# Performance work log

Measured on AMD Instinct MI355X. Metric: run time of the kernel, lower is better.

The kernel has to match this reference:

```python
import jax, jax.numpy as jnp
import numpy as np

T, B, H, L = 512, 128, 256, 2  # seq_len, batch, hidden(=input) size, num_layers


def setup_inputs() -> dict:
    key = jax.random.key(0)
    k0, k1, k2, k3, k4 = jax.random.split(key, 5)
    s = 1.0 / np.sqrt(H)  # PyTorch LSTM init range
    x = jax.random.normal(k0, (T, B, H), jnp.float32)
    W_ih = jax.random.uniform(k1, (L, 4 * H, H), jnp.float32, -s, s)
    W_hh = jax.random.uniform(k2, (L, 4 * H, H), jnp.float32, -s, s)
    b_ih = jax.random.uniform(k3, (L, 4 * H), jnp.float32, -s, s)
    b_hh = jax.random.uniform(k4, (L, 4 * H), jnp.float32, -s, s)
    return {"x": x, "W_ih": W_ih, "W_hh": W_hh, "b_ih": b_ih, "b_hh": b_hh}


def _lstm(x, W_ih, W_hh, b_ih, b_hh):
    Ln, fourH, _ = W_ih.shape
    Hh = fourH // 4
    Bn = x.shape[1]
    h0 = jnp.zeros((Ln, Bn, Hh), x.dtype)
    c0 = jnp.zeros((Ln, Bn, Hh), x.dtype)

    def step(carry, x_t):
        h, c = carry
        inp = x_t
        hs, cs = [], []
        for l in range(Ln):  # small static layer loop
            gates = inp @ W_ih[l].T + b_ih[l] + h[l] @ W_hh[l].T + b_hh[l]
            gi, gf, gg, go = jnp.split(gates, 4, axis=-1)
            gi = jax.nn.sigmoid(gi)
            gf = jax.nn.sigmoid(gf)
            gg = jnp.tanh(gg)
            go = jax.nn.sigmoid(go)
            c_new = gf * c[l] + gi * gg
            h_new = go * jnp.tanh(c_new)
            hs.append(h_new)
            cs.append(c_new)
            inp = h_new
        return (jnp.stack(hs), jnp.stack(cs)), inp

    (hT, cT), out = jax.lax.scan(step, (h0, c0), x)
    return out, hT, cT


def reference(x, W_ih, W_hh, b_ih, b_hh):
    # Returns (output [T,B,H], h_n [L,B,H], c_n [L,B,H]) as in DPLSTM.forward
    return _lstm(x, W_ih, W_hh, b_ih, b_hh)
```

## Files before the change

### kernel.cpp

```cpp
#include <hip/hip_runtime.h>
#include <math.h>

#define T_LEN 512
#define BATCH 128
#define HID   256
#define BH    (BATCH*HID)

__device__ __forceinline__ float sigmoid_f(float v) {
    return 1.f / (1.f + __expf(-v));
}
__device__ __forceinline__ float tanh_f(float v) {
    v = fminf(fmaxf(v, -15.f), 15.f);
    float e = __expf(2.f * v);
    return (e - 1.f) / (e + 1.f);
}
__device__ __forceinline__ float4 ldf4(const float* p) {
    return *reinterpret_cast<const float4*>(p);
}
__device__ __forceinline__ void fma4(float4& a, const float4 v, const float4 w) {
    a.x = fmaf(v.x, w.x, a.x);
    a.y = fmaf(v.y, w.y, a.y);
    a.z = fmaf(v.z, w.z, a.z);
    a.w = fmaf(v.w, w.w, a.w);
}
__device__ __forceinline__ float hsum4(const float4 a) {
    return (a.x + a.y) + (a.z + a.w);
}
__device__ __forceinline__ void pin4(float4& v) {
    asm volatile("" : "+v"(v.x), "+v"(v.y), "+v"(v.z), "+v"(v.w));
}
__device__ __forceinline__ void astore(float* p, float v) {
    __hip_atomic_store(p, v, __ATOMIC_RELAXED, __HIP_MEMORY_SCOPE_AGENT);
}
__device__ __forceinline__ float2 af2(const float* p) {
    unsigned long long u = __hip_atomic_load((const unsigned long long*)p,
                                             __ATOMIC_RELAXED, __HIP_MEMORY_SCOPE_AGENT);
    union { unsigned long long u; float2 f; } c; c.u = u;
    return c.f;
}
__device__ __forceinline__ float4 af4(const float* p) {
    const float2 a = af2(p), b = af2(p + 2);
    return make_float4(a.x, a.y, b.x, b.y);
}
template<int CTRL>
__device__ __forceinline__ float dpp_mv(float x) {
    return __int_as_float(__builtin_amdgcn_update_dpp(
        0, __float_as_int(x), CTRL, 0xF, 0xF, true));
}
__device__ __forceinline__ float red16(float x) {
    x += dpp_mv<0x111>(x);
    x += dpp_mv<0x112>(x);
    x += dpp_mv<0x114>(x);
    x += dpp_mv<0x118>(x);
    return x;
}

__global__ __launch_bounds__(256)
__attribute__((amdgpu_waves_per_eu(2, 2)))
void lstm_persist(
    const float* __restrict__ x,
    const float* __restrict__ Wih, const float* __restrict__ Whh,
    const float* __restrict__ bih, const float* __restrict__ bhh,
    float* __restrict__ out,
    float* __restrict__ h0buf,
    float* __restrict__ h1buf,
    int* __restrict__ flags)
{
    __shared__ float ls_in[8 * 576];
    __shared__ float ls_a [128 * 4];
    __shared__ float ls_ax[128 * 4];
    __shared__ float ls_c [128];

    const int tid = threadIdx.x;
    const int bid = blockIdx.x;
    const int bg = bid & 15;
    const int layer = (bid >> 4) & 1;
    const int jt = bid >> 5;
    const int jp = tid >> 4;
    const int kc = tid & 15;
    const int j = jt * 16 + jp;
    const int Bg0 = bg * 8;

    const float* Wih_l = Wih + (size_t)layer * 4 * HID * HID;
    const float* Whh_l = Whh + (size_t)layer * 4 * HID * HID;
    const float* bih_l = bih + layer * 4 * HID;
    const float* bhh_l = bhh + layer * 4 * HID;

    float4 wih[4][4], whh[4][4];
    float bias[4];
    #pragma unroll
    for (int g = 0; g < 4; ++g) {
        const int row = g * HID + j;
        const float* pih = Wih_l + (size_t)row * HID + kc * 16;
        const float* phh = Whh_l + (size_t)row * HID + kc * 16;
        #pragma unroll
        for (int m = 0; m < 4; ++m) {
            wih[g][m] = ldf4(pih + m * 4);
            pin4(wih[g][m]);
            whh[g][m] = ldf4(phh + m * 4);
            pin4(whh[g][m]);
        }
        bias[g] = bih_l[row] + bhh_l[row];
        asm volatile("" : "+v"(bias[g]));
    }

    if (tid < 128) ls_c[tid] = 0.f;

    int* myflag = flags + bg * 32 + layer * 16 + jt;

    #pragma unroll 1
    for (int s = 0; s <= T_LEN + 2; ++s) {
        if (s > 0 && tid < 32) {
            const int thr = (layer == 0 && tid >= 16) ? (s - 1) : s;
            const int* f = flags + bg * 32 + tid;
            while (__hip_atomic_load(f, __ATOMIC_RELAXED, __HIP_MEMORY_SCOPE_AGENT) < thr)
                __builtin_amdgcn_s_sleep(1);
        }
        __syncthreads();

        const bool crit = (layer == 0) ? (s >= 1 && s <= T_LEN) : (s >= 3);
        const bool xact = (layer == 0) ? (s < T_LEN) : (s >= 2 && s <= T_LEN + 1);
        const bool zeroh = (layer == 0) ? (s == 1) : (s == 3);

        if (crit || xact) {
            const float* ph0 = h0buf + (size_t)((s + 1) % 3) * BH;
            const float* ph1 = h1buf + (size_t)((s + 2) % 3) * BH;
            #pragma unroll
            for (int i = 0; i < 4; ++i) {
                const int F = tid + 256 * i;
                const int b = F >> 7;
                const int rr = F & 127;
                const int col = (rr & 63) * 4;
                const size_t row = (size_t)(Bg0 + b) * HID + col;
                float4 v = make_float4(0.f, 0.f, 0.f, 0.f);
                if ((rr >> 6) == 0) {
                    if (xact)
                        v = (layer == 0) ? ldf4(x + (size_t)s * BH + row)
                                         : af4(ph0 + row);
                } else if (crit && !zeroh) {
                    v = (layer == 0) ? af4(ph0 + row) : af4(ph1 + row);
                }
                *(float4*)(ls_in + b * 576 + (rr >> 3) * 36 + (rr & 7) * 4) = v;
            }
        }
        __syncthreads();

        if (crit) {
            #pragma unroll 2
            for (int b = 0; b < 8; ++b) {
                const float4* Lp = (const float4*)(ls_in + b * 576 + 288
                                                   + (kc >> 1) * 36 + (kc & 1) * 16);
                float4 in[4];
                #pragma unroll
                for (int m = 0; m < 4; ++m) in[m] = Lp[m];
                float4 ac[4];
                #pragma unroll
                for (int g = 0; g < 4; ++g) ac[g] = make_float4(0.f, 0.f, 0.f, 0.f);
                #pragma unroll
                for (int m = 0; m < 4; ++m) {
                    #pragma unroll
                    for (int g = 0; g < 4; ++g) fma4(ac[g], in[m], whh[g][m]);
                }
                const float a0 = red16(hsum4(ac[0]));
                const float a1 = red16(hsum4(ac[1]));
                const float a2 = red16(hsum4(ac[2]));
                const float a3 = red16(hsum4(ac[3]));
                if (kc == 15) {
                    const int cell = b * 16 + jp;
                    const float* axp = ls_ax + cell * 4;
                    float* ap = ls_a + cell * 4;
                    ap[0] = a0 + bias[0] + axp[0];
                    ap[1] = a1 + bias[1] + axp[1];
                    ap[2] = a2 + bias[2] + axp[2];
                    ap[3] = a3 + bias[3] + axp[3];
                }
            }
        }
        __syncthreads();

        if (crit && tid < 128) {
            const int bb = tid >> 4;
            const int jpp = tid & 15;
            const int t = (layer == 0) ? (s - 1) : (s - 3);
            float* hst = (layer == 0) ? (h0buf + (size_t)((s + 2) % 3) * BH)
                                      : (h1buf + (size_t)(s % 3) * BH);
            const bool last = (t == T_LEN - 1);
            const float* ap = ls_a + tid * 4;
            const float gi = sigmoid_f(ap[0]);
            const float gf = sigmoid_f(ap[1]);
            const float gg = tanh_f   (ap[2]);
            const float go = sigmoid_f(ap[3]);
            const float cold = ls_c[tid];
            const float cnew = fmaf(gf, cold, gi * gg);
            ls_c[tid] = cnew;
            const float h = go * tanh_f(cnew);
            const int B = Bg0 + bb;
            const int jg = jt * 16 + jpp;
            astore(hst + (size_t)B * HID + jg, h);
            if (layer == 1)
                out[(size_t)t * BH + (size_t)B * HID + jg] = h;
            if (last) {
                float* hn  = out + (size_t)T_LEN * BH;
                float* cnp = hn + 2 * BH;
                hn [(size_t)layer * BH + (size_t)B * HID + jg] = h;
                cnp[(size_t)layer * BH + (size_t)B * HID + jg] = cnew;
            }
        }
        __syncthreads();
        if (s <= T_LEN + 1 && tid == 0)
            __hip_atomic_store(myflag, s + 1, __ATOMIC_RELAXED, __HIP_MEMORY_SCOPE_AGENT);

        if (xact) {
            #pragma unroll 2
            for (int b = 0; b < 8; ++b) {
                const float4* Lp = (const float4*)(ls_in + b * 576
                                                   + (kc >> 1) * 36 + (kc & 1) * 16);
                float4 in[4];
                #pragma unroll
                for (int m = 0; m < 4; ++m) in[m] = Lp[m];
                float4 ac[4];
                #pragma unroll
                for (int g = 0; g < 4; ++g) ac[g] = make_float4(0.f, 0.f, 0.f, 0.f);
                #pragma unroll
                for (int m = 0; m < 4; ++m) {
                    #pragma unroll
                    for (int g = 0; g < 4; ++g) fma4(ac[g], in[m], wih[g][m]);
                }
                const float a0 = red16(hsum4(ac[0]));
                const float a1 = red16(hsum4(ac[1]));
                const float a2 = red16(hsum4(ac[2]));
                const float a3 = red16(hsum4(ac[3]));
                if (kc == 15) {
                    float* axp = ls_ax + (b * 16 + jp) * 4;
                    axp[0] = a0;
                    axp[1] = a1;
                    axp[2] = a2;
                    axp[3] = a3;
                }
            }
        }
    }
}

extern "C" void kernel_launch(void* const* d_in, const int* in_sizes, int n_in,
                              void* d_out, int out_size, void* d_ws, size_t ws_size,
                              hipStream_t stream) {
    const float* x   = (const float*)d_in[0];
    const float* Wih = (const float*)d_in[1];
    const float* Whh = (const float*)d_in[2];
    const float* bih = (const float*)d_in[3];
    const float* bhh = (const float*)d_in[4];
    float* out = (float*)d_out;

    float* h0 = (float*)d_ws;
    float* h1 = h0 + 3 * BH;
    int* flags = (int*)(h1 + 3 * BH);

    hipLaunchKernelGGL(lstm_persist, dim3(512), dim3(256), 0, stream,
                       x, Wih, Whh, bih, bhh, out, h0, h1, flags);
}
```

Baseline: 3.624 ms.

## Fuse gate activation into recurrent matvec, keep state in registers, remap blocks to XCDs

Fuses the LSTM cell update into the recurrent matvec loop. The reducing lane now computes the activations and c/h directly, which drops the LDS gate buffers and one block barrier per step. The input projection partial sums and the cell state stay in per-thread registers. Weights are moved into AGPRs through accvgpr writes, and the divisions are replaced by rcp with one Newton step. Block IDs are remapped so blocks of the same batch group spread across XCDs. The cost is higher register pressure, and the AGPR operands may need to be copied back to VGPRs before each FMA.

```diff
diff --git a/kernel.cpp b/kernel.cpp
--- a/kernel.cpp
+++ b/kernel.cpp
@@ -6,13 +6,17 @@
 #define HID   256
 #define BH    (BATCH*HID)
 
+__device__ __forceinline__ float frcp(float d) {
+    float r = __builtin_amdgcn_rcpf(d);
+    return r * fmaf(-d, r, 2.0f);
+}
 __device__ __forceinline__ float sigmoid_f(float v) {
-    return 1.f / (1.f + __expf(-v));
+    return frcp(1.f + __expf(-v));
 }
 __device__ __forceinline__ float tanh_f(float v) {
     v = fminf(fmaxf(v, -15.f), 15.f);
-    float e = __expf(2.f * v);
-    return (e - 1.f) / (e + 1.f);
+    const float e = __expf(2.f * v);
+    return (e - 1.f) * frcp(e + 1.f);
 }
 __device__ __forceinline__ float4 ldf4(const float* p) {
     return *reinterpret_cast<const float4*>(p);
@@ -26,8 +30,15 @@
 __device__ __forceinline__ float hsum4(const float4 a) {
     return (a.x + a.y) + (a.z + a.w);
 }
-__device__ __forceinline__ void pin4(float4& v) {
-    asm volatile("" : "+v"(v.x), "+v"(v.y), "+v"(v.z), "+v"(v.w));
+__device__ __forceinline__ float agpr(float v) {
+    float a;
+    asm("v_accvgpr_write_b32 %0, %1" : "=a"(a) : "v"(v));
+    return a;
+}
+__device__ __forceinline__ float4 agpr4(const float4 v) {
+    float4 r;
+    r.x = agpr(v.x); r.y = agpr(v.y); r.z = agpr(v.z); r.w = agpr(v.w);
+    return r;
 }
 __device__ __forceinline__ void astore(float* p, float v) {
     __hip_atomic_store(p, v, __ATOMIC_RELAXED, __HIP_MEMORY_SCOPE_AGENT);
@@ -67,15 +78,15 @@
     int* __restrict__ flags)
 {
     __shared__ float ls_in[8 * 576];
-    __shared__ float ls_a [128 * 4];
-    __shared__ float ls_ax[128 * 4];
-    __shared__ float ls_c [128];
 
     const int tid = threadIdx.x;
     const int bid = blockIdx.x;
-    const int bg = bid & 15;
-    const int layer = (bid >> 4) & 1;
-    const int jt = bid >> 5;
+    const int xcd = bid & 7;
+    const int kk  = bid >> 3;
+    const int g_  = xcd + 8 * (kk & 3);
+    const int bg  = kk >> 2;
+    const int layer = g_ >> 4;
+    const int jt  = g_ & 15;
     const int jp = tid >> 4;
     const int kc = tid & 15;
     const int j = jt * 16 + jp;
@@ -95,16 +106,21 @@
         const float* phh = Whh_l + (size_t)row * HID + kc * 16;
         #pragma unroll
         for (int m = 0; m < 4; ++m) {
-            wih[g][m] = ldf4(pih + m * 4);
-            pin4(wih[g][m]);
-            whh[g][m] = ldf4(phh + m * 4);
-            pin4(whh[g][m]);
+            wih[g][m] = agpr4(ldf4(pih + m * 4));
+            whh[g][m] = agpr4(ldf4(phh + m * 4));
         }
         bias[g] = bih_l[row] + bhh_l[row];
         asm volatile("" : "+v"(bias[g]));
     }
 
-    if (tid < 128) ls_c[tid] = 0.f;
+    float c_reg[8];
+    float ax[8][4];
+    #pragma unroll
+    for (int b = 0; b < 8; ++b) {
+        c_reg[b] = 0.f;
+        #pragma unroll
+        for (int g = 0; g < 4; ++g) ax[b][g] = 0.f;
+    }
 
     int* myflag = flags + bg * 32 + layer * 16 + jt;
 
@@ -145,65 +161,50 @@
         }
         __syncthreads();
 
+        const int lofs = (kc >> 1) * 36 + (kc & 1) * 16;
+
         if (crit) {
-            #pragma unroll 2
-            for (int b = 0; b < 8; ++b) {
-                const float4* Lp = (const float4*)(ls_in + b * 576 + 288
-                                                   + (kc >> 1) * 36 + (kc & 1) * 16);
-                float4 in[4];
-                #pragma unroll
-                for (int m = 0; m < 4; ++m) in[m] = Lp[m];
-                float4 ac[4];
-                #pragma unroll
-                for (int g = 0; g < 4; ++g) ac[g] = make_float4(0.f, 0.f, 0.f, 0.f);
-                #pragma unroll
-                for (int m = 0; m < 4; ++m) {
-                    #pragma unroll
-                    for (int g = 0; g < 4; ++g) fma4(ac[g], in[m], whh[g][m]);
-                }
-                const float a0 = red16(hsum4(ac[0]));
-                const float a1 = red16(hsum4(ac[1]));
-                const float a2 = red16(hsum4(ac[2]));
-                const float a3 = red16(hsum4(ac[3]));
-                if (kc == 15) {
-                    const int cell = b * 16 + jp;
-                    const float* axp = ls_ax + cell * 4;
-                    float* ap = ls_a + cell * 4;
-                    ap[0] = a0 + bias[0] + axp[0];
-                    ap[1] = a1 + bias[1] + axp[1];
-                    ap[2] = a2 + bias[2] + axp[2];
-                    ap[3] = a3 + bias[3] + axp[3];
-                }
-            }
-        }
-        __syncthreads();
-
-        if (crit && tid < 128) {
-            const int bb = tid >> 4;
-            const int jpp = tid & 15;
             const int t = (layer == 0) ? (s - 1) : (s - 3);
             float* hst = (layer == 0) ? (h0buf + (size_t)((s + 2) % 3) * BH)
                                       : (h1buf + (size_t)(s % 3) * BH);
             const bool last = (t == T_LEN - 1);
-            const float* ap = ls_a + tid * 4;
-            const float gi = sigmoid_f(ap[0]);
-            const float gf = sigmoid_f(ap[1]);
-            const float gg = tanh_f   (ap[2]);
-            const float go = sigmoid_f(ap[3]);
-            const float cold = ls_c[tid];
-            const float cnew = fmaf(gf, cold, gi * gg);
-            ls_c[tid] = cnew;
-            const float h = go * tanh_f(cnew);
-            const int B = Bg0 + bb;
-            const int jg = jt * 16 + jpp;
-            astore(hst + (size_t)B * HID + jg, h);
-            if (layer == 1)
-                out[(size_t)t * BH + (size_t)B * HID + jg] = h;
-            if (last) {
-                float* hn  = out + (size_t)T_LEN * BH;
-                float* cnp = hn + 2 * BH;
-                hn [(size_t)layer * BH + (size_t)B * HID + jg] = h;
-                cnp[(size_t)layer * BH + (size_t)B * HID + jg] = cnew;
+            #pragma unroll
+            for (int b = 0; b < 8; ++b) {
+                const float4* Lp = (const float4*)(ls_in + b * 576 + 288 + lofs);
+                float4 i0 = Lp[0], i1 = Lp[1], i2 = Lp[2], i3 = Lp[3];
+                float4 ac[4];
+                #pragma unroll
+                for (int g = 0; g < 4; ++g) ac[g] = make_float4(0.f, 0.f, 0.f, 0.f);
+                #pragma unroll
+                for (int g = 0; g < 4; ++g) {
+                    fma4(ac[g], i0, whh[g][0]);
+                    fma4(ac[g], i1, whh[g][1]);
+                    fma4(ac[g], i2, whh[g][2]);
+                    fma4(ac[g], i3, whh[g][3]);
+                }
+                const float r0 = red16(hsum4(ac[0]) + ax[b][0]);
+                const float r1 = red16(hsum4(ac[1]) + ax[b][1]);
+                const float r2 = red16(hsum4(ac[2]) + ax[b][2]);
+                const float r3 = red16(hsum4(ac[3]) + ax[b][3]);
+                if (kc == 15) {
+                    const float gi = sigmoid_f(r0 + bias[0]);
+                    const float gf = sigmoid_f(r1 + bias[1]);
+                    const float gg = tanh_f   (r2 + bias[2]);
+                    const float go = sigmoid_f(r3 + bias[3]);
+                    const float cnew = fmaf(gf, c_reg[b], gi * gg);
+                    c_reg[b] = cnew;
+                    const float h = go * tanh_f(cnew);
+                    const int B = Bg0 + b;
+                    astore(hst + (size_t)B * HID + j, h);
+                    if (layer == 1)
+                        out[(size_t)t * BH + (size_t)B * HID + j] = h;
+                    if (last) {
+                        float* hn  = out + (size_t)T_LEN * BH;
+                        float* cnp = hn + 2 * BH;
+                        hn [(size_t)layer * BH + (size_t)B * HID + j] = h;
+                        cnp[(size_t)layer * BH + (size_t)B * HID + j] = cnew;
+                    }
+                }
             }
         }
         __syncthreads();
@@ -211,32 +212,22 @@
             __hip_atomic_store(myflag, s + 1, __ATOMIC_RELAXED, __HIP_MEMORY_SCOPE_AGENT);
 
         if (xact) {
-            #pragma unroll 2
+            #pragma unroll
             for (int b = 0; b < 8; ++b) {
-                const float4* Lp = (const float4*)(ls_in + b * 576
-                                                   + (kc >> 1) * 36 + (kc & 1) * 16);
-                float4 in[4];
-                #pragma unroll
-                for (int m = 0; m < 4; ++m) in[m] = Lp[m];
+                const float4* Lp = (const float4*)(ls_in + b * 576 + lofs);
+                float4 i0 = Lp[0], i1 = Lp[1], i2 = Lp[2], i3 = Lp[3];
                 float4 ac[4];
                 #pragma unroll
                 for (int g = 0; g < 4; ++g) ac[g] = make_float4(0.f, 0.f, 0.f, 0.f);
                 #pragma unroll
-                for (int m = 0; m < 4; ++m) {
-                    #pragma unroll
-                    for (int g = 0; g < 4; ++g) fma4(ac[g], in[m], wih[g][m]);
-                }
-                const float a0 = red16(hsum4(ac[0]));
-                const float a1 = red16(hsum4(ac[1]));
-                const float a2 = red16(hsum4(ac[2]));
-                const float a3 = red16(hsum4(ac[3]));
-                if (kc == 15) {
-                    float* axp = ls_ax + (b * 16 + jp) * 4;
-                    axp[0] = a0;
-                    axp[1] = a1;
-                    axp[2] = a2;
-                    axp[3] = a3;
-                }
+                for (int g = 0; g < 4; ++g) {
+                    fma4(ac[g], i0, wih[g][0]);
+                    fma4(ac[g], i1, wih[g][1]);
+                    fma4(ac[g], i2, wih[g][2]);
+                    fma4(ac[g], i3, wih[g][3]);
+                }
+                #pragma unroll
+                for (int g = 0; g < 4; ++g) ax[b][g] = hsum4(ac[g]);
             }
         }
     }
```

Result: slower. 4.557 ms (+25.7%).
